# Kernel tuning notes

Measured on AMD Instinct MI355X. Metric: run time of the kernel, lower is better.

Reference implementation:

```python
import jax, jax.numpy as jnp
import numpy as np

DECAY = 0.99
EPS = 1e-05


def setup_inputs() -> dict:
    key = jax.random.key(0)
    k1, k2, k3, k4 = jax.random.split(key, 4)
    B, T, D, V = 8, 2048, 256, 8192
    return {
        "input": jax.random.normal(k1, (B, T, D), dtype=jnp.float32),
        "embed": jax.random.normal(k2, (V, D), dtype=jnp.float32),
        "cluster_size": jax.random.uniform(k3, (V,), dtype=jnp.float32),
        "embed_avg": jax.random.normal(k4, (V, D), dtype=jnp.float32),
    }


def reference(input, embed, cluster_size, embed_avg):
    # input: [B,T,D]; embed: [V,D]
    B, T, D = input.shape
    V = embed.shape[0]
    # squared euclidean distances (argmin identical to cdist argmin)
    d2 = (
        jnp.sum(input * input, axis=-1, keepdims=True)
        - 2.0 * jnp.einsum("btd,vd->btv", input, embed)
        + jnp.sum(embed * embed, axis=-1)
    )  # [B,T,V]
    codes = jnp.argmin(d2, axis=-1)  # [B,T] int
    quantize = jnp.take(embed, codes, axis=0)  # [B,T,D]

    # EMA codebook update (training-mode buffer update, faithful to update_embed)
    flat_codes = codes.reshape(-1)  # [B*T]
    flat_x = input.reshape(-1, D)
    counts = jax.ops.segment_sum(
        jnp.ones_like(flat_codes, dtype=input.dtype), flat_codes, num_segments=V
    )  # onehot.sum(0) over all B*T tokens
    # codebook = mean over T of per-timestep onehot^T @ x == segment_sum / T
    codebook = jax.ops.segment_sum(flat_x, flat_codes, num_segments=V) / T  # [V,D]
    new_cluster_size = cluster_size * DECAY + counts * (1.0 - DECAY)
    new_embed_avg = embed_avg * DECAY + codebook * (1.0 - DECAY)
    new_embed = new_embed_avg / (new_cluster_size + EPS)[:, None]

    # straight-through estimator
    quantize = input + jax.lax.stop_gradient(quantize - input)
    return quantize, codes, new_embed, new_cluster_size, new_embed_avg
```

## Files before the change

kernel.cpp:

```cpp
#include <hip/hip_runtime.h>
#include <math.h>

#define M_TOK 16384
#define DIM   256
#define VOC   8192

#define BM 128
#define BN 128
#define NBLK_N (VOC / BN)
#define GAP_EPS 1.5f

typedef unsigned short u16;
typedef unsigned long long u64;
typedef __attribute__((ext_vector_type(8))) __bf16 bf16x8;
typedef __attribute__((ext_vector_type(4))) float f32x4;

#define WS_ESQ      0
#define WS_CANDV    40960
#define WS_CANDI    1089536
#define WS_CANDS    2138112
#define WS_XHI      3186688
#define WS_EHI      7380992
#define WS_COUNTS   9478144
#define WS_SUMS     9486336
#define WS_ZERO_OFF_BYTES ((size_t)WS_COUNTS * 4)
#define WS_ZERO_BYTES     ((size_t)(8192 + 2097152 + 16) * 4)

#define OUT_Q   0
#define OUT_C   4194304
#define OUT_NE  4210688
#define OUT_NCS 6307840
#define OUT_NEA 6316032

__device__ inline u16 f2bf_rn(float x) {
    unsigned u = __float_as_uint(x);
    unsigned r = u + 0x7FFFu + ((u >> 16) & 1u);
    return (u16)(r >> 16);
}
__device__ inline unsigned f2key(float f) {
    unsigned b = __float_as_uint(f);
    return (b & 0x80000000u) ? ~b : (b | 0x80000000u);
}
__device__ inline float key2f(unsigned k) {
    unsigned b = (k & 0x80000000u) ? (k ^ 0x80000000u) : ~k;
    return __uint_as_float(b);
}

__global__ __launch_bounds__(256) void prep_kernel(
    const float* __restrict__ X, const float* __restrict__ E,
    u16* __restrict__ Xhi, u16* __restrict__ Ehi,
    float* __restrict__ esq)
{
    int row  = blockIdx.x * 4 + (threadIdx.x >> 6);
    int lane = threadIdx.x & 63;
    bool isX = row < M_TOK;
    int r = isX ? row : row - M_TOK;
    const float* src = isX ? X + (size_t)row * DIM : E + (size_t)r * DIM;
    float4 v = ((const float4*)src)[lane];

    ushort4 h;
    h.x = f2bf_rn(v.x); h.y = f2bf_rn(v.y);
    h.z = f2bf_rn(v.z); h.w = f2bf_rn(v.w);
    u16* dh = isX ? Xhi : Ehi;
    *(ushort4*)&dh[(size_t)r * DIM + lane * 4] = h;

    if (!isX) {
        float s = v.x * v.x + v.y * v.y + v.z * v.z + v.w * v.w;
        #pragma unroll
        for (int o = 1; o < 64; o <<= 1) s += __shfl_xor(s, o, 64);
        if (lane == 0) esq[r] = s;
    }
}

__global__ __launch_bounds__(256, 2) void mfma_argmin_kernel(
    const u16* __restrict__ Xhi, const u16* __restrict__ Ehi,
    const float* __restrict__ esq,
    float* __restrict__ candV, int* __restrict__ candI, float* __restrict__ candS)
{
    __shared__ __align__(16) char tiles[4 * 8192];

    const int tid = threadIdx.x;
    const int w = tid >> 6, l = tid & 63;
    const int wy = w >> 1, wx = w & 1;
    const int m0 = blockIdx.x * BM;
    const int n0 = blockIdx.y * BN;

    f32x4 acc[4][4];
    #pragma unroll
    for (int i = 0; i < 4; ++i)
        #pragma unroll
        for (int j = 0; j < 4; ++j) acc[i][j] = (f32x4)0.0f;

    const u16* gbase = (w < 2) ? Xhi : Ehi;
    const int row0   = (w < 2) ? m0 : n0;
    const int koff   = (w & 1) * 32;
    const int swz_c = (l & 3) ^ ((l >> 3) & 3);
    const u16* gsrc0 = gbase + (size_t)(row0 + (l >> 2)) * DIM + koff + swz_c * 8;
    char* ltile = tiles + w * 8192;

    const int frow = l & 15, fq = l >> 4;
    const int fs = ((fq ^ ((frow >> 1) & 3)) * 16);
    const char* a0P = tiles + 0 * 8192 + (wy * 64 + frow) * 64 + fs;
    const char* a1P = tiles + 1 * 8192 + (wy * 64 + frow) * 64 + fs;
    const char* b0P = tiles + 2 * 8192 + (wx * 64 + frow) * 64 + fs;
    const char* b1P = tiles + 3 * 8192 + (wx * 64 + frow) * 64 + fs;

    for (int ks = 0; ks < 4; ++ks) {
        const int k0 = ks * 64;
        __syncthreads();
        #pragma unroll
        for (int i = 0; i < 8; ++i) {
            __builtin_amdgcn_global_load_lds(
                (const __attribute__((address_space(1))) unsigned int*)(gsrc0 + (size_t)i * 16 * DIM + k0),
                (__attribute__((address_space(3))) unsigned int*)(ltile + i * 1024),
                16, 0, 0);
        }
        __syncthreads();

        bf16x8 a0[4], a1[4];
        #pragma unroll
        for (int mt = 0; mt < 4; ++mt) {
            a0[mt] = *(const bf16x8*)(a0P + mt * 1024);
            a1[mt] = *(const bf16x8*)(a1P + mt * 1024);
        }
        #pragma unroll
        for (int nt = 0; nt < 4; ++nt) {
            bf16x8 b0 = *(const bf16x8*)(b0P + nt * 1024);
            bf16x8 b1 = *(const bf16x8*)(b1P + nt * 1024);
            #pragma unroll
            for (int mt = 0; mt < 4; ++mt) {
                acc[mt][nt] = __builtin_amdgcn_mfma_f32_16x16x32_bf16(a0[mt], b0, acc[mt][nt], 0, 0, 0);
                acc[mt][nt] = __builtin_amdgcn_mfma_f32_16x16x32_bf16(a1[mt], b1, acc[mt][nt], 0, 0, 0);
            }
        }
    }

    __syncthreads();
    float* smB = (float*)tiles;
    int*   smI = (int*)(tiles + 1024);
    float* smS = (float*)(tiles + 2048);

    float eq[4];
    #pragma unroll
    for (int nt = 0; nt < 4; ++nt) eq[nt] = esq[n0 + wx * 64 + nt * 16 + frow];

    #pragma unroll
    for (int mt = 0; mt < 4; ++mt) {
        #pragma unroll
        for (int r = 0; r < 4; ++r) {
            float b = 3.4e38f, s = 3.4e38f;
            int bi = 0;
            #pragma unroll
            for (int nt = 0; nt < 4; ++nt) {
                float v = fmaf(-2.0f, acc[mt][nt][r], eq[nt]);
                int col = n0 + wx * 64 + nt * 16 + frow;
                if (v < b) { s = b; b = v; bi = col; }
                else if (v < s) s = v;
            }
            #pragma unroll
            for (int o = 1; o < 16; o <<= 1) {
                float ob = __shfl_xor(b, o, 64);
                int   oi = __shfl_xor(bi, o, 64);
                float os = __shfl_xor(s, o, 64);
                bool take = (ob < b) || (ob == b && oi < bi);
                float keep = take ? b : ob;
                b  = take ? ob : b;
                bi = take ? oi : bi;
                s  = fminf(fminf(s, os), keep);
            }
            if (frow == 0) {
                int m_loc = wy * 64 + mt * 16 + fq * 4 + r;
                smB[wx * 128 + m_loc] = b;
                smI[wx * 128 + m_loc] = bi;
                smS[wx * 128 + m_loc] = s;
            }
        }
    }
    __syncthreads();
    if (tid < 128) {
        float b0 = smB[tid],       b1 = smB[128 + tid];
        int   i0 = smI[tid],       i1 = smI[128 + tid];
        float s0 = smS[tid],       s1 = smS[128 + tid];
        bool take = (b1 < b0);
        float b = take ? b1 : b0;
        int  bi = take ? i1 : i0;
        float s = fminf(fminf(s0, s1), take ? b0 : b1);
        size_t e = (size_t)blockIdx.y * M_TOK + (m0 + tid);
        candV[e] = b; candI[e] = bi; candS[e] = s;
    }
}

__global__ __launch_bounds__(256) void post_kernel(
    const float* __restrict__ X, const float* __restrict__ E,
    const float* __restrict__ esq,
    const float* __restrict__ candV, const int* __restrict__ candI,
    const float* __restrict__ candS,
    float* __restrict__ out_q, float* __restrict__ out_codes,
    float* __restrict__ counts, float* __restrict__ sums)
{
    const int lane = threadIdx.x & 63;
    const int wv   = threadIdx.x >> 6;
    const int row0 = blockIdx.x * 16 + wv * 4;
    for (int rr = 0; rr < 4; ++rr) {
        const int row = row0 + rr;
        float bv = candV[(size_t)lane * M_TOK + row];
        float bs = candS[(size_t)lane * M_TOK + row];
        int   bi = candI[(size_t)lane * M_TOK + row];

        u64 pk = ((u64)f2key(bv) << 32) | (unsigned)bi;
        u64 m = pk;
        #pragma unroll
        for (int o = 1; o < 64; o <<= 1) {
            u64 other = __shfl_xor(m, o, 64);
            m = (other < m) ? other : m;
        }
        float best = key2f((unsigned)(m >> 32));
        int   code = (int)(unsigned)(m & 0xFFFFFFFFull);

        float sec = (pk == m) ? bs : bv;
        #pragma unroll
        for (int o = 1; o < 64; o <<= 1) sec = fminf(sec, __shfl_xor(sec, o, 64));

        const float4 x4 = ((const float4*)&X[(size_t)row * DIM])[lane];

        if (sec - best < GAP_EPS) {
            const float bound = best + GAP_EPS;
            float bestV = 3.4e38f;
            int   bestI = 0x7FFFFFFF;
            u64 mask = __ballot(bv < bound);
            while (mask) {
                int src = __ffsll((unsigned long long)mask) - 1;
                mask &= mask - 1;
                int c = __shfl(bi, src, 64);
                float4 e4 = ((const float4*)&E[(size_t)c * DIM])[lane];
                float d = x4.x * e4.x + x4.y * e4.y + x4.z * e4.z + x4.w * e4.w;
                #pragma unroll
                for (int o = 1; o < 64; o <<= 1) d += __shfl_xor(d, o, 64);
                float v = fmaf(-2.0f, d, esq[c]);
                if (v < bestV || (v == bestV && c < bestI)) { bestV = v; bestI = c; }
            }
            u64 dmask = __ballot(bs < bound);
            while (dmask) {
                int e = __ffsll((unsigned long long)dmask) - 1;
                dmask &= dmask - 1;
                const int c0 = e * BN;
                for (int j = 0; j < BN; j += 4) {
                    float4 e0 = ((const float4*)&E[(size_t)(c0 + j + 0) * DIM])[lane];
                    float4 e1 = ((const float4*)&E[(size_t)(c0 + j + 1) * DIM])[lane];
                    float4 e2 = ((const float4*)&E[(size_t)(c0 + j + 2) * DIM])[lane];
                    float4 e3 = ((const float4*)&E[(size_t)(c0 + j + 3) * DIM])[lane];
                    float d0 = x4.x * e0.x + x4.y * e0.y + x4.z * e0.z + x4.w * e0.w;
                    float d1 = x4.x * e1.x + x4.y * e1.y + x4.z * e1.z + x4.w * e1.w;
                    float d2 = x4.x * e2.x + x4.y * e2.y + x4.z * e2.z + x4.w * e2.w;
                    float d3 = x4.x * e3.x + x4.y * e3.y + x4.z * e3.z + x4.w * e3.w;
                    #pragma unroll
                    for (int o = 1; o < 64; o <<= 1) {
                        d0 += __shfl_xor(d0, o, 64);
                        d1 += __shfl_xor(d1, o, 64);
                        d2 += __shfl_xor(d2, o, 64);
                        d3 += __shfl_xor(d3, o, 64);
                    }
                    float v0 = fmaf(-2.0f, d0, esq[c0 + j + 0]);
                    float v1 = fmaf(-2.0f, d1, esq[c0 + j + 1]);
                    float v2 = fmaf(-2.0f, d2, esq[c0 + j + 2]);
                    float v3 = fmaf(-2.0f, d3, esq[c0 + j + 3]);
                    if (v0 < bestV || (v0 == bestV && c0 + j + 0 < bestI)) { bestV = v0; bestI = c0 + j + 0; }
                    if (v1 < bestV || (v1 == bestV && c0 + j + 1 < bestI)) { bestV = v1; bestI = c0 + j + 1; }
                    if (v2 < bestV || (v2 == bestV && c0 + j + 2 < bestI)) { bestV = v2; bestI = c0 + j + 2; }
                    if (v3 < bestV || (v3 == bestV && c0 + j + 3 < bestI)) { bestV = v3; bestI = c0 + j + 3; }
                }
            }
            code = bestI;
        }

        if (lane == 0) {
            out_codes[row] = (float)code;
            atomicAdd(&counts[code], 1.0f);
        }
        float4 e4 = ((const float4*)&E[(size_t)code * DIM])[lane];
        float4 q;
        q.x = x4.x + (e4.x - x4.x);
        q.y = x4.y + (e4.y - x4.y);
        q.z = x4.z + (e4.z - x4.z);
        q.w = x4.w + (e4.w - x4.w);
        ((float4*)&out_q[(size_t)row * DIM])[lane] = q;
        float* s = &sums[(size_t)code * DIM + lane * 4];
        atomicAdd(s + 0, x4.x);
        atomicAdd(s + 1, x4.y);
        atomicAdd(s + 2, x4.z);
        atomicAdd(s + 3, x4.w);
    }
}

__global__ __launch_bounds__(256) void finalize_kernel(
    const float* __restrict__ cs, const float* __restrict__ ea,
    const float* __restrict__ counts, const float* __restrict__ sums,
    float* __restrict__ out_embed, float* __restrict__ out_cs,
    float* __restrict__ out_ea)
{
    int vd = blockIdx.x * 256 + threadIdx.x;
    int v = vd >> 8, d = vd & 255;
    float cnt = counts[v];
    float ncs = cs[v] * 0.99f + cnt * 0.01f;
    float cb  = sums[vd] * (1.0f / 2048.0f);
    float nea = ea[vd] * 0.99f + cb * 0.01f;
    out_ea[vd] = nea;
    out_embed[vd] = nea / (ncs + 1e-5f);
    if (d == 0) out_cs[v] = ncs;
}

extern "C" void kernel_launch(void* const* d_in, const int* in_sizes, int n_in,
                              void* d_out, int out_size, void* d_ws, size_t ws_size,
                              hipStream_t stream)
{
    const float* input     = (const float*)d_in[0];
    const float* embed     = (const float*)d_in[1];
    const float* cluster   = (const float*)d_in[2];
    const float* embed_avg = (const float*)d_in[3];

    float* out = (float*)d_out;
    float* ws  = (float*)d_ws;

    float* esq      = ws + WS_ESQ;
    float* candV    = ws + WS_CANDV;
    int*   candI    = (int*)(ws + WS_CANDI);
    float* candS    = ws + WS_CANDS;
    u16*   Xhi      = (u16*)(ws + WS_XHI);
    u16*   Ehi      = (u16*)(ws + WS_EHI);
    float* counts   = ws + WS_COUNTS;
    float* sums     = ws + WS_SUMS;

    hipMemsetAsync((char*)d_ws + WS_ZERO_OFF_BYTES, 0, WS_ZERO_BYTES, stream);

    prep_kernel<<<(M_TOK + VOC) / 4, 256, 0, stream>>>(
        input, embed, Xhi, Ehi, esq);

    dim3 g1(M_TOK / BM, VOC / BN);
    mfma_argmin_kernel<<<g1, 256, 0, stream>>>(
        Xhi, Ehi, esq, candV, candI, candS);

    post_kernel<<<M_TOK / 16, 256, 0, stream>>>(
        input, embed, esq, candV, candI, candS,
        out + OUT_Q, out + OUT_C, counts, sums);

    finalize_kernel<<<(VOC * DIM) / 256, 256, 0, stream>>>(
        cluster, embed_avg, counts, sums,
        out + OUT_NE, out + OUT_NCS, out + OUT_NEA);
}
```

Before: 334.2 us.

## Swap MFMA operands for row-local argmin and transpose candidate layout

```diff
diff --git a/kernel.cpp b/kernel.cpp
--- a/kernel.cpp
+++ b/kernel.cpp
@@ -129,8 +129,8 @@
             bf16x8 b1 = *(const bf16x8*)(b1P + nt * 1024);
             #pragma unroll
             for (int mt = 0; mt < 4; ++mt) {
-                acc[mt][nt] = __builtin_amdgcn_mfma_f32_16x16x32_bf16(a0[mt], b0, acc[mt][nt], 0, 0, 0);
-                acc[mt][nt] = __builtin_amdgcn_mfma_f32_16x16x32_bf16(a1[mt], b1, acc[mt][nt], 0, 0, 0);
+                acc[mt][nt] = __builtin_amdgcn_mfma_f32_16x16x32_bf16(b0, a0[mt], acc[mt][nt], 0, 0, 0);
+                acc[mt][nt] = __builtin_amdgcn_mfma_f32_16x16x32_bf16(b1, a1[mt], acc[mt][nt], 0, 0, 0);
             }
         }
     }
@@ -140,40 +140,44 @@
     int*   smI = (int*)(tiles + 1024);
     float* smS = (float*)(tiles + 2048);
 
-    float eq[4];
-    #pragma unroll
-    for (int nt = 0; nt < 4; ++nt) eq[nt] = esq[n0 + wx * 64 + nt * 16 + frow];
+    float eqv[16];
+    #pragma unroll
+    for (int nt = 0; nt < 4; ++nt) {
+        float4 t = *(const float4*)&esq[n0 + wx * 64 + nt * 16 + fq * 4];
+        eqv[nt * 4 + 0] = t.x; eqv[nt * 4 + 1] = t.y;
+        eqv[nt * 4 + 2] = t.z; eqv[nt * 4 + 3] = t.w;
+    }
 
     #pragma unroll
     for (int mt = 0; mt < 4; ++mt) {
-        #pragma unroll
-        for (int r = 0; r < 4; ++r) {
-            float b = 3.4e38f, s = 3.4e38f;
-            int bi = 0;
+        float b = 3.4e38f, s = 3.4e38f;
+        int bi = 0;
+        #pragma unroll
+        for (int nt = 0; nt < 4; ++nt) {
             #pragma unroll
-            for (int nt = 0; nt < 4; ++nt) {
-                float v = fmaf(-2.0f, acc[mt][nt][r], eq[nt]);
-                int col = n0 + wx * 64 + nt * 16 + frow;
-                if (v < b) { s = b; b = v; bi = col; }
+            for (int r = 0; r < 4; ++r) {
+                float v = fmaf(-2.0f, acc[mt][nt][r], eqv[nt * 4 + r]);
+                int c = n0 + wx * 64 + nt * 16 + fq * 4 + r;
+                if (v < b) { s = b; b = v; bi = c; }
                 else if (v < s) s = v;
             }
-            #pragma unroll
-            for (int o = 1; o < 16; o <<= 1) {
-                float ob = __shfl_xor(b, o, 64);
-                int   oi = __shfl_xor(bi, o, 64);
-                float os = __shfl_xor(s, o, 64);
-                bool take = (ob < b) || (ob == b && oi < bi);
-                float keep = take ? b : ob;
-                b  = take ? ob : b;
-                bi = take ? oi : bi;
-                s  = fminf(fminf(s, os), keep);
-            }
-            if (frow == 0) {
-                int m_loc = wy * 64 + mt * 16 + fq * 4 + r;
-                smB[wx * 128 + m_loc] = b;
-                smI[wx * 128 + m_loc] = bi;
-                smS[wx * 128 + m_loc] = s;
-            }
+        }
+        #pragma unroll
+        for (int o = 16; o < 64; o <<= 1) {
+            float ob = __shfl_xor(b, o, 64);
+            int   oi = __shfl_xor(bi, o, 64);
+            float os = __shfl_xor(s, o, 64);
+            bool take = (ob < b) || (ob == b && oi < bi);
+            float keep = take ? b : ob;
+            b  = take ? ob : b;
+            bi = take ? oi : bi;
+            s  = fminf(fminf(s, os), keep);
+        }
+        if (l < 16) {
+            int m_loc = wy * 64 + mt * 16 + l;
+            smB[wx * 128 + m_loc] = b;
+            smI[wx * 128 + m_loc] = bi;
+            smS[wx * 128 + m_loc] = s;
         }
     }
     __syncthreads();
@@ -185,7 +189,7 @@
         float b = take ? b1 : b0;
         int  bi = take ? i1 : i0;
         float s = fminf(fminf(s0, s1), take ? b0 : b1);
-        size_t e = (size_t)blockIdx.y * M_TOK + (m0 + tid);
+        size_t e = (size_t)(m0 + tid) * NBLK_N + blockIdx.y;
         candV[e] = b; candI[e] = bi; candS[e] = s;
     }
 }
@@ -199,97 +203,94 @@
     float* __restrict__ counts, float* __restrict__ sums)
 {
     const int lane = threadIdx.x & 63;
-    const int wv   = threadIdx.x >> 6;
-    const int row0 = blockIdx.x * 16 + wv * 4;
-    for (int rr = 0; rr < 4; ++rr) {
-        const int row = row0 + rr;
-        float bv = candV[(size_t)lane * M_TOK + row];
-        float bs = candS[(size_t)lane * M_TOK + row];
-        int   bi = candI[(size_t)lane * M_TOK + row];
-
-        u64 pk = ((u64)f2key(bv) << 32) | (unsigned)bi;
-        u64 m = pk;
-        #pragma unroll
-        for (int o = 1; o < 64; o <<= 1) {
-            u64 other = __shfl_xor(m, o, 64);
-            m = (other < m) ? other : m;
-        }
-        float best = key2f((unsigned)(m >> 32));
-        int   code = (int)(unsigned)(m & 0xFFFFFFFFull);
-
-        float sec = (pk == m) ? bs : bv;
-        #pragma unroll
-        for (int o = 1; o < 64; o <<= 1) sec = fminf(sec, __shfl_xor(sec, o, 64));
-
-        const float4 x4 = ((const float4*)&X[(size_t)row * DIM])[lane];
-
-        if (sec - best < GAP_EPS) {
-            const float bound = best + GAP_EPS;
-            float bestV = 3.4e38f;
-            int   bestI = 0x7FFFFFFF;
-            u64 mask = __ballot(bv < bound);
-            while (mask) {
-                int src = __ffsll((unsigned long long)mask) - 1;
-                mask &= mask - 1;
-                int c = __shfl(bi, src, 64);
-                float4 e4 = ((const float4*)&E[(size_t)c * DIM])[lane];
-                float d = x4.x * e4.x + x4.y * e4.y + x4.z * e4.z + x4.w * e4.w;
+    const int row  = blockIdx.x * 4 + (threadIdx.x >> 6);
+
+    float bv = candV[(size_t)row * NBLK_N + lane];
+    float bs = candS[(size_t)row * NBLK_N + lane];
+    int   bi = candI[(size_t)row * NBLK_N + lane];
+
+    u64 pk = ((u64)f2key(bv) << 32) | (unsigned)bi;
+    u64 m = pk;
+    #pragma unroll
+    for (int o = 1; o < 64; o <<= 1) {
+        u64 other = __shfl_xor(m, o, 64);
+        m = (other < m) ? other : m;
+    }
+    float best = key2f((unsigned)(m >> 32));
+    int   code = (int)(unsigned)(m & 0xFFFFFFFFull);
+
+    float sec = (pk == m) ? bs : bv;
+    #pragma unroll
+    for (int o = 1; o < 64; o <<= 1) sec = fminf(sec, __shfl_xor(sec, o, 64));
+
+    const float4 x4 = ((const float4*)&X[(size_t)row * DIM])[lane];
+
+    if (sec - best < GAP_EPS) {
+        const float bound = best + GAP_EPS;
+        float bestV = 3.4e38f;
+        int   bestI = 0x7FFFFFFF;
+        u64 mask = __ballot(bv < bound);
+        while (mask) {
+            int src = __ffsll((unsigned long long)mask) - 1;
+            mask &= mask - 1;
+            int c = __shfl(bi, src, 64);
+            float4 e4 = ((const float4*)&E[(size_t)c * DIM])[lane];
+            float d = x4.x * e4.x + x4.y * e4.y + x4.z * e4.z + x4.w * e4.w;
+            #pragma unroll
+            for (int o = 1; o < 64; o <<= 1) d += __shfl_xor(d, o, 64);
+            float v = fmaf(-2.0f, d, esq[c]);
+            if (v < bestV || (v == bestV && c < bestI)) { bestV = v; bestI = c; }
+        }
+        u64 dmask = __ballot(bs < bound);
+        while (dmask) {
+            int e = __ffsll((unsigned long long)dmask) - 1;
+            dmask &= dmask - 1;
+            const int c0 = e * BN;
+            for (int j = 0; j < BN; j += 4) {
+                float4 e0 = ((const float4*)&E[(size_t)(c0 + j + 0) * DIM])[lane];
+                float4 e1 = ((const float4*)&E[(size_t)(c0 + j + 1) * DIM])[lane];
+                float4 e2 = ((const float4*)&E[(size_t)(c0 + j + 2) * DIM])[lane];
+                float4 e3 = ((const float4*)&E[(size_t)(c0 + j + 3) * DIM])[lane];
+                float d0 = x4.x * e0.x + x4.y * e0.y + x4.z * e0.z + x4.w * e0.w;
+                float d1 = x4.x * e1.x + x4.y * e1.y + x4.z * e1.z + x4.w * e1.w;
+                float d2 = x4.x * e2.x + x4.y * e2.y + x4.z * e2.z + x4.w * e2.w;
+                float d3 = x4.x * e3.x + x4.y * e3.y + x4.z * e3.z + x4.w * e3.w;
                 #pragma unroll
-                for (int o = 1; o < 64; o <<= 1) d += __shfl_xor(d, o, 64);
-                float v = fmaf(-2.0f, d, esq[c]);
-                if (v < bestV || (v == bestV && c < bestI)) { bestV = v; bestI = c; }
+                for (int o = 1; o < 64; o <<= 1) {
+                    d0 += __shfl_xor(d0, o, 64);
+                    d1 += __shfl_xor(d1, o, 64);
+                    d2 += __shfl_xor(d2, o, 64);
+                    d3 += __shfl_xor(d3, o, 64);
+                }
+                float v0 = fmaf(-2.0f, d0, esq[c0 + j + 0]);
+                float v1 = fmaf(-2.0f, d1, esq[c0 + j + 1]);
+                float v2 = fmaf(-2.0f, d2, esq[c0 + j + 2]);
+                float v3 = fmaf(-2.0f, d3, esq[c0 + j + 3]);
+                if (v0 < bestV || (v0 == bestV && c0 + j + 0 < bestI)) { bestV = v0; bestI = c0 + j + 0; }
+                if (v1 < bestV || (v1 == bestV && c0 + j + 1 < bestI)) { bestV = v1; bestI = c0 + j + 1; }
+                if (v2 < bestV || (v2 == bestV && c0 + j + 2 < bestI)) { bestV = v2; bestI = c0 + j + 2; }
+                if (v3 < bestV || (v3 == bestV && c0 + j + 3 < bestI)) { bestV = v3; bestI = c0 + j + 3; }
             }
-            u64 dmask = __ballot(bs < bound);
-            while (dmask) {
-                int e = __ffsll((unsigned long long)dmask) - 1;
-                dmask &= dmask - 1;
-                const int c0 = e * BN;
-                for (int j = 0; j < BN; j += 4) {
-                    float4 e0 = ((const float4*)&E[(size_t)(c0 + j + 0) * DIM])[lane];
-                    float4 e1 = ((const float4*)&E[(size_t)(c0 + j + 1) * DIM])[lane];
-                    float4 e2 = ((const float4*)&E[(size_t)(c0 + j + 2) * DIM])[lane];
-                    float4 e3 = ((const float4*)&E[(size_t)(c0 + j + 3) * DIM])[lane];
-                    float d0 = x4.x * e0.x + x4.y * e0.y + x4.z * e0.z + x4.w * e0.w;
-                    float d1 = x4.x * e1.x + x4.y * e1.y + x4.z * e1.z + x4.w * e1.w;
-                    float d2 = x4.x * e2.x + x4.y * e2.y + x4.z * e2.z + x4.w * e2.w;
-                    float d3 = x4.x * e3.x + x4.y * e3.y + x4.z * e3.z + x4.w * e3.w;
-                    #pragma unroll
-                    for (int o = 1; o < 64; o <<= 1) {
-                        d0 += __shfl_xor(d0, o, 64);
-                        d1 += __shfl_xor(d1, o, 64);
-                        d2 += __shfl_xor(d2, o, 64);
-                        d3 += __shfl_xor(d3, o, 64);
-                    }
-                    float v0 = fmaf(-2.0f, d0, esq[c0 + j + 0]);
-                    float v1 = fmaf(-2.0f, d1, esq[c0 + j + 1]);
-                    float v2 = fmaf(-2.0f, d2, esq[c0 + j + 2]);
-                    float v3 = fmaf(-2.0f, d3, esq[c0 + j + 3]);
-                    if (v0 < bestV || (v0 == bestV && c0 + j + 0 < bestI)) { bestV = v0; bestI = c0 + j + 0; }
-                    if (v1 < bestV || (v1 == bestV && c0 + j + 1 < bestI)) { bestV = v1; bestI = c0 + j + 1; }
-                    if (v2 < bestV || (v2 == bestV && c0 + j + 2 < bestI)) { bestV = v2; bestI = c0 + j + 2; }
-                    if (v3 < bestV || (v3 == bestV && c0 + j + 3 < bestI)) { bestV = v3; bestI = c0 + j + 3; }
-                }
-            }
-            code = bestI;
-        }
-
-        if (lane == 0) {
-            out_codes[row] = (float)code;
-            atomicAdd(&counts[code], 1.0f);
-        }
-        float4 e4 = ((const float4*)&E[(size_t)code * DIM])[lane];
-        float4 q;
-        q.x = x4.x + (e4.x - x4.x);
-        q.y = x4.y + (e4.y - x4.y);
-        q.z = x4.z + (e4.z - x4.z);
-        q.w = x4.w + (e4.w - x4.w);
-        ((float4*)&out_q[(size_t)row * DIM])[lane] = q;
-        float* s = &sums[(size_t)code * DIM + lane * 4];
-        atomicAdd(s + 0, x4.x);
-        atomicAdd(s + 1, x4.y);
-        atomicAdd(s + 2, x4.z);
-        atomicAdd(s + 3, x4.w);
-    }
+        }
+        code = bestI;
+    }
+
+    if (lane == 0) {
+        out_codes[row] = (float)code;
+        atomicAdd(&counts[code], 1.0f);
+    }
+    float4 e4 = ((const float4*)&E[(size_t)code * DIM])[lane];
+    float4 q;
+    q.x = x4.x + (e4.x - x4.x);
+    q.y = x4.y + (e4.y - x4.y);
+    q.z = x4.z + (e4.z - x4.z);
+    q.w = x4.w + (e4.w - x4.w);
+    ((float4*)&out_q[(size_t)row * DIM])[lane] = q;
+    float* s = &sums[(size_t)code * DIM + lane * 4];
+    atomicAdd(s + 0, x4.x);
+    atomicAdd(s + 1, x4.y);
+    atomicAdd(s + 2, x4.z);
+    atomicAdd(s + 3, x4.w);
 }
 
 __global__ __launch_bounds__(256) void finalize_kernel(
@@ -339,7 +340,7 @@
     mfma_argmin_kernel<<<g1, 256, 0, stream>>>(
         Xhi, Ehi, esq, candV, candI, candS);
 
-    post_kernel<<<M_TOK / 16, 256, 0, stream>>>(
+    post_kernel<<<M_TOK / 4, 256, 0, stream>>>(
         input, embed, esq, candV, candI, candS,
         out + OUT_Q, out + OUT_C, counts, sums);
 
```

Result: faster. 301.9 us (-9.7%).
